# Kernel optimization log

Measured on AMD Instinct MI355X. Metric: run time of the kernel, lower is better.

Reference implementation:

```python
import jax, jax.numpy as jnp
import numpy as np

NUM_CODES = 8192
DIM = 512
COMMITMENT_COST = 0.25


def setup_inputs() -> dict:
    key = jax.random.key(0)
    kx, kc = jax.random.split(key)
    x = jax.random.normal(kx, (8, 4096, DIM), dtype=jnp.float32)
    # nn.init.uniform_(codebook.weight, -1/num_codes, 1/num_codes)
    bound = 1.0 / NUM_CODES
    codebook = jax.random.uniform(kc, (NUM_CODES, DIM), dtype=jnp.float32,
                                  minval=-bound, maxval=bound)
    return {"x": x, "codebook": codebook}


def reference(x, codebook):
    orig_shape = x.shape
    flat = x.reshape(-1, orig_shape[-1])              # [N, D]
    # Squared-distance expansion (argmin-equivalent to torch.cdist's L2):
    # ||f||^2 - 2 f.c + ||c||^2
    x_sq = jnp.sum(flat * flat, axis=-1, keepdims=True)          # [N, 1]
    c_sq = jnp.sum(codebook * codebook, axis=-1)                 # [K]
    dists = x_sq - 2.0 * jnp.einsum('nd,kd->nk', flat, codebook) + c_sq  # [N, K]
    indices_flat = jnp.argmin(dists, axis=-1)                    # [N] int
    quantized_flat = codebook[indices_flat]                      # [N, D]
    # codebook_loss = mse(quantized, sg(flat)); commitment = mse(flat, sg(quantized))
    codebook_loss = jnp.mean((quantized_flat - jax.lax.stop_gradient(flat)) ** 2)
    commitment_loss = jnp.mean((flat - jax.lax.stop_gradient(quantized_flat)) ** 2)
    vq_loss = codebook_loss + COMMITMENT_COST * commitment_loss
    # straight-through
    quantized_st = flat + jax.lax.stop_gradient(quantized_flat - flat)
    return (quantized_st.reshape(orig_shape), vq_loss,
            indices_flat.reshape(orig_shape[:-1]))
```

## Files before the change

### kernel.cpp

```cpp
#include <hip/hip_runtime.h>


#define NROWS 32768
#define KCODES 8192
#define DD 512
#define CAP 24
#define MARGIN 2.5e-4f

typedef __bf16 bf16_t;
typedef __bf16 bf16x8 __attribute__((ext_vector_type(8)));
typedef float f32x4 __attribute__((ext_vector_type(4)));

__device__ __forceinline__ void gld16(const bf16_t* g, bf16_t* l) {
  __builtin_amdgcn_global_load_lds(
      (const __attribute__((address_space(1))) void*)g,
      (__attribute__((address_space(3))) void*)l, 16, 0, 0);
}

__global__ __launch_bounds__(256) void prep_kernel(const float* __restrict__ in,
                                                   float* __restrict__ out_sq,
                                                   bf16_t* __restrict__ outb,
                                                   int nrows) {
  const int wave = threadIdx.x >> 6;
  const int lane = threadIdx.x & 63;
  const int row = blockIdx.x * 4 + wave;
  if (row >= nrows) return;
  const float* p = in + (size_t)row * DD;
  double s = 0.0;
#pragma unroll
  for (int j = 0; j < DD / 64; ++j) {
    float v = p[j * 64 + lane];
    float sq = v * v;
    s += (double)sq;
  }
  for (int off = 32; off > 0; off >>= 1) s += __shfl_down(s, off, 64);
  if (lane == 0) out_sq[row] = (float)s;
  const float4* p4 = (const float4*)p;
  float4 a = p4[lane * 2];
  float4 b = p4[lane * 2 + 1];
  bf16x8 o = {(bf16_t)a.x, (bf16_t)a.y, (bf16_t)a.z, (bf16_t)a.w,
              (bf16_t)b.x, (bf16_t)b.y, (bf16_t)b.z, (bf16_t)b.w};
  *(bf16x8*)(outb + (size_t)row * DD + lane * 8) = o;
}

__global__ __launch_bounds__(256, 2) void coarse_kernel(
    const bf16_t* __restrict__ xbf, const bf16_t* __restrict__ cbbf,
    const float* __restrict__ csq, unsigned char* __restrict__ cnt_g,
    unsigned short* __restrict__ list_g, unsigned* __restrict__ bmin_g) {
  __shared__ bf16_t As[128 * 128];
  __shared__ bf16_t Bs[128 * 128];
  __shared__ unsigned best[128];
  __shared__ int cnt_l[128];
  __shared__ unsigned short list_l[128 * CAP];

  const int tid = threadIdx.x;
  const int w = tid >> 6;
  const int lane = tid & 63;
  const int q = lane >> 4;
  const int l15 = lane & 15;
  const int rOff = (w & 1) * 64;
  const int cOff = (w >> 1) * 64;

  const int bid = blockIdx.x;
  const int xcd = bid & 7;
  const int g = bid >> 3;
  const int qtr = xcd >> 1;
  const int rowblk = (xcd & 1) * 128 + g;
  const int row0 = rowblk * 128;
  const int cbase = qtr * (KCODES / 4);
  const int NCI = (KCODES / 4) / 128;

  for (int i = tid; i < 128; i += 256) { best[i] = 0xFFFFFFFFu; cnt_l[i] = 0; }

  const int sxrow = tid >> 4;
  const int spos = tid & 15;
  const int sg = spos ^ (sxrow & 7);
  const bf16_t* aGb = xbf + (size_t)(row0 + sxrow) * DD + sg * 8;
  const bf16_t* bGb = cbbf + (size_t)(cbase + sxrow) * DD + sg * 8;
  bf16_t* aLb = As + tid * 8;
  bf16_t* bLb = Bs + tid * 8;

  const int rm = l15 & 7;
  const int arb0 = (rOff + l15) * 128;
  const int brb0 = (cOff + l15) * 128;

  __syncthreads();

  f32x4 acc[4][4];

#pragma unroll 1
  for (int ci = 0; ci < NCI; ++ci) {
    const int c0 = cbase + ci * 128;
    const size_t cioff = (size_t)(ci * 128) * DD;
#pragma unroll
    for (int rt = 0; rt < 4; ++rt)
#pragma unroll
      for (int ct = 0; ct < 4; ++ct) {
        f32x4 z = {0.f, 0.f, 0.f, 0.f};
        acc[rt][ct] = z;
      }

#pragma unroll 1
    for (int kc = 0; kc < DD / 128; ++kc) {
      const int kb = kc * 128;
      __syncthreads();
#pragma unroll
      for (int c = 0; c < 8; ++c) {
        gld16(aGb + kb + c * (16 * DD), aLb + c * 2048);
        gld16(bGb + cioff + kb + c * (16 * DD), bLb + c * 2048);
      }
      __syncthreads();

#pragma unroll
      for (int ks = 0; ks < 4; ++ks) {
        const int kqx = ((ks * 4 + q) ^ rm) << 3;
        bf16x8 af[4], bfr[4];
#pragma unroll
        for (int rt = 0; rt < 4; ++rt)
          af[rt] = *(const bf16x8*)&As[arb0 + rt * (16 * 128) + kqx];
#pragma unroll
        for (int ct = 0; ct < 4; ++ct)
          bfr[ct] = *(const bf16x8*)&Bs[brb0 + ct * (16 * 128) + kqx];
#pragma unroll
        for (int rt = 0; rt < 4; ++rt)
#pragma unroll
          for (int ct = 0; ct < 4; ++ct)
            acc[rt][ct] = __builtin_amdgcn_mfma_f32_16x16x32_bf16(
                af[rt], bfr[ct], acc[rt][ct], 0, 0, 0);
      }
    }

    float cs1[4];
#pragma unroll
    for (int ct = 0; ct < 4; ++ct)
      cs1[ct] = 1.0f + csq[c0 + cOff + ct * 16 + l15];

#pragma unroll
    for (int rt = 0; rt < 4; ++rt) {
#pragma unroll
      for (int reg = 0; reg < 4; ++reg) {
        float m = fmaf(-2.0f, acc[rt][0][reg], cs1[0]);
#pragma unroll
        for (int ct = 1; ct < 4; ++ct) {
          float d = fmaf(-2.0f, acc[rt][ct][reg], cs1[ct]);
          m = fminf(m, d);
        }
        unsigned mb = __float_as_uint(m);
#pragma unroll
        for (int msk = 1; msk <= 8; msk <<= 1) {
          unsigned o = __shfl_xor(mb, msk, 64);
          mb = mb < o ? mb : o;
        }
        if (l15 == 0) atomicMin(&best[rOff + rt * 16 + q * 4 + reg], mb);
      }
    }
    __syncthreads();

#pragma unroll
    for (int rt = 0; rt < 4; ++rt) {
#pragma unroll
      for (int reg = 0; reg < 4; ++reg) {
        const int rloc = rOff + rt * 16 + q * 4 + reg;
        const float thr = __uint_as_float(best[rloc]) + MARGIN;
#pragma unroll
        for (int ct = 0; ct < 4; ++ct) {
          float d = fmaf(-2.0f, acc[rt][ct][reg], cs1[ct]);
          if (d <= thr) {
            int pos2 = atomicAdd(&cnt_l[rloc], 1);
            if (pos2 < CAP)
              list_l[rloc * CAP + pos2] =
                  (unsigned short)(c0 + cOff + ct * 16 + l15);
          }
        }
      }
    }
  }

  __syncthreads();

  for (int i = tid; i < 128; i += 256) {
    int c = cnt_l[i];
    cnt_g[(size_t)(row0 + i) * 4 + qtr] = (unsigned char)(c > CAP ? CAP + 1 : c);
    bmin_g[(size_t)(row0 + i) * 4 + qtr] = best[i];
  }
  for (int i = tid; i < 128 * CAP; i += 256) {
    const int r = i / CAP, p = i % CAP;
    list_g[((size_t)(row0 + r) * 4 + qtr) * CAP + p] = list_l[i];
  }
}

__device__ __forceinline__ float exact_dist(const float4* __restrict__ xr4,
                                            const float* __restrict__ cb,
                                            const float* __restrict__ csq,
                                            float xs, int idx) {
  const float4* cr4 = (const float4*)(cb + (size_t)idx * DD);
  float acc = 0.0f;
  for (int k4 = 0; k4 < DD / 4; ++k4) {
    float4 xv = xr4[k4];
    float4 cv = cr4[k4];
    acc = fmaf(xv.x, cv.x, acc);
    acc = fmaf(xv.y, cv.y, acc);
    acc = fmaf(xv.z, cv.z, acc);
    acc = fmaf(xv.w, cv.w, acc);
  }
  float t = xs - 2.0f * acc;
  return t + csq[idx];
}

__global__ __launch_bounds__(256) void rescore_epilogue_kernel(
    const float* __restrict__ x, const float* __restrict__ cb,
    const float* __restrict__ xsq, const float* __restrict__ csq,
    const unsigned short* __restrict__ list,
    const unsigned char* __restrict__ cnt, const unsigned* __restrict__ bmin,
    float* __restrict__ out_q, float* __restrict__ out_idx_f,
    double* __restrict__ partials) {
  const int row = blockIdx.x * 4 + (threadIdx.x >> 6);
  const int lane = threadIdx.x & 63;
  const unsigned char* c4 = cnt + (size_t)row * 4;
  const unsigned* bm4 = bmin + (size_t)row * 4;
  const float xs = xsq[row];
  const float4* xr4 = (const float4*)(x + (size_t)row * DD);

  float qm[4];
  int n[4];
#pragma unroll
  for (int s = 0; s < 4; ++s) {
    qm[s] = __uint_as_float(bm4[s]);
    n[s] = c4[s];
  }
  const float gmin = fminf(fminf(qm[0], qm[1]), fminf(qm[2], qm[3]));
  const float cut = gmin + MARGIN;
  bool listed[4], scanq[4];
  int L = 0;
#pragma unroll
  for (int s = 0; s < 4; ++s) {
    const bool rel = (qm[s] <= cut);
    listed[s] = rel && (n[s] <= CAP);
    scanq[s] = rel && (n[s] > CAP);
    if (listed[s]) L += n[s];
  }
  if (L > 64) {
#pragma unroll
    for (int s = 0; s < 4; ++s)
      if (listed[s]) { listed[s] = false; scanq[s] = true; }
    L = 0;
  }

  unsigned long long bestv = ~0ULL;

  int myidx = -1;
  int base = 0;
#pragma unroll
  for (int s = 0; s < 4; ++s) {
    if (listed[s]) {
      if (myidx < 0 && lane >= base && lane < base + n[s])
        myidx = (int)list[((size_t)row * 4 + s) * CAP + (lane - base)];
      base += n[s];
    }
  }
  if (myidx >= 0) {
    float d = exact_dist(xr4, cb, csq, xs, myidx);
    bestv = ((unsigned long long)__float_as_uint(d) << 32) | (unsigned)myidx;
  }

#pragma unroll
  for (int s = 0; s < 4; ++s) {
    if (scanq[s]) {
      const int q0 = s * (KCODES / 4);
      for (int idx = q0 + lane; idx < q0 + KCODES / 4; idx += 64) {
        float d = exact_dist(xr4, cb, csq, xs, idx);
        unsigned long long pk =
            ((unsigned long long)__float_as_uint(d) << 32) | (unsigned)idx;
        if (pk < bestv) bestv = pk;
      }
    }
  }

#pragma unroll
  for (int s = 1; s <= 32; s <<= 1) {
    unsigned long long o = __shfl_xor(bestv, s, 64);
    if (o < bestv) bestv = o;
  }
  const int k = (int)(bestv & 0xffffffffu);

  const float4* qr = (const float4*)(cb + (size_t)k * DD);
  float4* orow = (float4*)(out_q + (size_t)row * DD);

  float4 xa = xr4[lane], qa = qr[lane];
  float dax = qa.x - xa.x, day = qa.y - xa.y, daz = qa.z - xa.z, daw = qa.w - xa.w;
  float4 oa;
  oa.x = xa.x + dax; oa.y = xa.y + day; oa.z = xa.z + daz; oa.w = xa.w + daw;
  orow[lane] = oa;
  double pa = (double)(dax * dax) + (double)(day * day) +
              (double)(daz * daz) + (double)(daw * daw);

  float4 xb = xr4[lane + 64], qb = qr[lane + 64];
  float dbx = qb.x - xb.x, dby = qb.y - xb.y, dbz = qb.z - xb.z, dbw = qb.w - xb.w;
  float4 ob;
  ob.x = xb.x + dbx; ob.y = xb.y + dby; ob.z = xb.z + dbz; ob.w = xb.w + dbw;
  orow[lane + 64] = ob;
  double pb = (double)(dbx * dbx) + (double)(dby * dby) +
              (double)(dbz * dbz) + (double)(dbw * dbw);

  for (int off = 32; off > 0; off >>= 1) pa += __shfl_down(pa, off, 64);
  for (int off = 32; off > 0; off >>= 1) pb += __shfl_down(pb, off, 64);
  if (lane == 0) {
    partials[row] = pa + pb;
    out_idx_f[row] = (float)k;
  }
}

__global__ __launch_bounds__(256) void finalize_kernel(
    const double* __restrict__ partials, float* __restrict__ out_loss) {
  __shared__ double red[256];
  double s = 0.0;
  for (int i = threadIdx.x; i < NROWS; i += 256) s += partials[i];
  red[threadIdx.x] = s;
  __syncthreads();
  for (int st = 128; st > 0; st >>= 1) {
    if (threadIdx.x < st) red[threadIdx.x] += red[threadIdx.x + st];
    __syncthreads();
  }
  if (threadIdx.x == 0) {
    double mean = red[0] / ((double)NROWS * (double)DD);
    float cl = (float)mean;
    out_loss[0] = cl + 0.25f * cl;
  }
}

extern "C" void kernel_launch(void* const* d_in, const int* in_sizes, int n_in,
                              void* d_out, int out_size, void* d_ws,
                              size_t ws_size, hipStream_t stream) {
  const float* x = (const float*)d_in[0];
  const float* cb = (const float*)d_in[1];
  float* out = (float*)d_out;

  char* ws = (char*)d_ws;
  double* partials = (double*)ws;
  float* csq = (float*)(ws + 262144);
  float* xsq = (float*)(ws + 262144 + 32768);
  unsigned char* cnt = (unsigned char*)(ws + 262144 + 32768 + 131072);
  unsigned* bmin = (unsigned*)(ws + 262144 + 32768 + 131072 + 131072);
  unsigned short* list =
      (unsigned short*)(ws + 262144 + 32768 + 131072 + 131072 + 524288);

  bf16_t* cbbf = (bf16_t*)d_out;
  bf16_t* xbf = cbbf + (size_t)KCODES * DD;

  prep_kernel<<<KCODES / 4, 256, 0, stream>>>(cb, csq, cbbf, KCODES);
  prep_kernel<<<NROWS / 4, 256, 0, stream>>>(x, xsq, xbf, NROWS);
  coarse_kernel<<<1024, 256, 0, stream>>>(xbf, cbbf, csq, cnt, list, bmin);
  rescore_epilogue_kernel<<<NROWS / 4, 256, 0, stream>>>(
      x, cb, xsq, csq, list, cnt, bmin, out, out + 16777216 + 1, partials);
  finalize_kernel<<<1, 256, 0, stream>>>(partials, out + 16777216);
}
```

Before: 878.6 us.

## Split LDS tiles into 64-wide halves with new swizzle; merge prep launches

The two prep kernel launches for codebook and input rows are merged into one launch that branches on block index. The coarse GEMM's shared-memory tiles are reorganised from 128-wide rows into two 64-element-wide halves, with a matching XOR swizzle for the global-to-LDS loads and the fragment reads. This aims to cut LDS bank conflicts and address arithmetic in the MFMA inner loop, and to save one launch. The total LDS footprint is unchanged, and the new swizzle indexing must line up exactly with the load pattern to stay correct.

```diff
diff --git a/kernel.cpp b/kernel.cpp
--- a/kernel.cpp
+++ b/kernel.cpp
@@ -17,14 +17,25 @@
       (__attribute__((address_space(3))) void*)l, 16, 0, 0);
 }
 
-__global__ __launch_bounds__(256) void prep_kernel(const float* __restrict__ in,
-                                                   float* __restrict__ out_sq,
-                                                   bf16_t* __restrict__ outb,
-                                                   int nrows) {
+__global__ __launch_bounds__(256) void prep_kernel(
+    const float* __restrict__ x, const float* __restrict__ cb,
+    float* __restrict__ xsq, float* __restrict__ csq,
+    bf16_t* __restrict__ xbf, bf16_t* __restrict__ cbbf) {
   const int wave = threadIdx.x >> 6;
   const int lane = threadIdx.x & 63;
-  const int row = blockIdx.x * 4 + wave;
-  if (row >= nrows) return;
+  const float* in;
+  float* osq;
+  bf16_t* ob;
+  int row;
+  if (blockIdx.x < KCODES / 4) {
+    in = cb; osq = csq; ob = cbbf;
+    row = blockIdx.x * 4 + wave;
+    if (row >= KCODES) return;
+  } else {
+    in = x; osq = xsq; ob = xbf;
+    row = (blockIdx.x - KCODES / 4) * 4 + wave;
+    if (row >= NROWS) return;
+  }
   const float* p = in + (size_t)row * DD;
   double s = 0.0;
 #pragma unroll
@@ -34,21 +45,21 @@
     s += (double)sq;
   }
   for (int off = 32; off > 0; off >>= 1) s += __shfl_down(s, off, 64);
-  if (lane == 0) out_sq[row] = (float)s;
+  if (lane == 0) osq[row] = (float)s;
   const float4* p4 = (const float4*)p;
   float4 a = p4[lane * 2];
   float4 b = p4[lane * 2 + 1];
   bf16x8 o = {(bf16_t)a.x, (bf16_t)a.y, (bf16_t)a.z, (bf16_t)a.w,
               (bf16_t)b.x, (bf16_t)b.y, (bf16_t)b.z, (bf16_t)b.w};
-  *(bf16x8*)(outb + (size_t)row * DD + lane * 8) = o;
+  *(bf16x8*)(ob + (size_t)row * DD + lane * 8) = o;
 }
 
 __global__ __launch_bounds__(256, 2) void coarse_kernel(
     const bf16_t* __restrict__ xbf, const bf16_t* __restrict__ cbbf,
     const float* __restrict__ csq, unsigned char* __restrict__ cnt_g,
     unsigned short* __restrict__ list_g, unsigned* __restrict__ bmin_g) {
-  __shared__ bf16_t As[128 * 128];
-  __shared__ bf16_t Bs[128 * 128];
+  __shared__ bf16_t As[2][128 * 64];
+  __shared__ bf16_t Bs[2][128 * 64];
   __shared__ unsigned best[128];
   __shared__ int cnt_l[128];
   __shared__ unsigned short list_l[128 * CAP];
@@ -72,17 +83,19 @@
 
   for (int i = tid; i < 128; i += 256) { best[i] = 0xFFFFFFFFu; cnt_l[i] = 0; }
 
-  const int sxrow = tid >> 4;
-  const int spos = tid & 15;
-  const int sg = spos ^ (sxrow & 7);
-  const bf16_t* aGb = xbf + (size_t)(row0 + sxrow) * DD + sg * 8;
-  const bf16_t* bGb = cbbf + (size_t)(cbase + sxrow) * DD + sg * 8;
-  bf16_t* aLb = As + tid * 8;
-  bf16_t* bLb = Bs + tid * 8;
+  const int srow = tid >> 3;
+  const int spos = tid & 7;
+  const int sg = spos ^ (srow & 7);
+  const bf16_t* aGb = xbf + (size_t)(row0 + srow) * DD + sg * 8;
+  const bf16_t* bGb = cbbf + (size_t)(cbase + srow) * DD + sg * 8;
 
   const int rm = l15 & 7;
-  const int arb0 = (rOff + l15) * 128;
-  const int brb0 = (cOff + l15) * 128;
+  int afb[4], bfb[4];
+#pragma unroll
+  for (int rt = 0; rt < 4; ++rt) {
+    afb[rt] = (rOff + rt * 16 + l15) * 64 + ((q ^ rm) << 3);
+    bfb[rt] = (cOff + rt * 16 + l15) * 64 + ((q ^ rm) << 3);
+  }
 
   __syncthreads();
 
@@ -105,22 +118,26 @@
       const int kb = kc * 128;
       __syncthreads();
 #pragma unroll
-      for (int c = 0; c < 8; ++c) {
-        gld16(aGb + kb + c * (16 * DD), aLb + c * 2048);
-        gld16(bGb + cioff + kb + c * (16 * DD), bLb + c * 2048);
-      }
+      for (int h = 0; h < 2; ++h)
+#pragma unroll
+        for (int j = 0; j < 4; ++j) {
+          gld16(aGb + kb + h * 64 + j * (32 * DD), &As[h][j * 2048 + tid * 8]);
+          gld16(bGb + cioff + kb + h * 64 + j * (32 * DD),
+                &Bs[h][j * 2048 + tid * 8]);
+        }
       __syncthreads();
 
 #pragma unroll
       for (int ks = 0; ks < 4; ++ks) {
-        const int kqx = ((ks * 4 + q) ^ rm) << 3;
+        const int h = ks >> 1;
+        const int sx = (ks & 1) << 5;
         bf16x8 af[4], bfr[4];
 #pragma unroll
         for (int rt = 0; rt < 4; ++rt)
-          af[rt] = *(const bf16x8*)&As[arb0 + rt * (16 * 128) + kqx];
+          af[rt] = *(const bf16x8*)&As[h][afb[rt] ^ sx];
 #pragma unroll
         for (int ct = 0; ct < 4; ++ct)
-          bfr[ct] = *(const bf16x8*)&Bs[brb0 + ct * (16 * 128) + kqx];
+          bfr[ct] = *(const bf16x8*)&Bs[h][bfb[ct] ^ sx];
 #pragma unroll
         for (int rt = 0; rt < 4; ++rt)
 #pragma unroll
@@ -347,8 +364,8 @@
   bf16_t* cbbf = (bf16_t*)d_out;
   bf16_t* xbf = cbbf + (size_t)KCODES * DD;
 
-  prep_kernel<<<KCODES / 4, 256, 0, stream>>>(cb, csq, cbbf, KCODES);
-  prep_kernel<<<NROWS / 4, 256, 0, stream>>>(x, xsq, xbf, NROWS);
+  prep_kernel<<<(KCODES + NROWS) / 4, 256, 0, stream>>>(x, cb, xsq, csq,
+                                                        xbf, cbbf);
   coarse_kernel<<<1024, 256, 0, stream>>>(xbf, cbbf, csq, cnt, list, bmin);
   rescore_epilogue_kernel<<<NROWS / 4, 256, 0, stream>>>(
       x, cb, xsq, csq, list, cnt, bmin, out, out + 16777216 + 1, partials);
```

After: 871.3 us. About the same (-0.8%).
